# Kernel tuning notes

Hardware: AMD Instinct MI355X
Metric: run time of the kernel (lower is better)

Reference implementation:

```python
import jax, jax.numpy as jnp
import numpy as np
import math


def _sinusoidal_pe(seq_len, hidden_dim, dtype):
    pos = jnp.arange(seq_len, dtype=jnp.float32)[:, None]              # [S,1]
    div = jnp.exp(jnp.arange(0, hidden_dim, 2, dtype=jnp.float32) * (-math.log(10000.0) / hidden_dim))  # [H/2]
    ang = pos * div                                                    # [S,H/2]
    pe = jnp.stack([jnp.sin(ang), jnp.cos(ang)], axis=-1).reshape(seq_len, hidden_dim)  # interleave sin/cos
    return pe.astype(dtype)


def setup_inputs() -> dict:
    key = jax.random.key(0)
    ks = jax.random.split(key, 12)
    B, S, H = 4, 2048, 1024
    scale = 1.0 / math.sqrt(H)
    inp = {
        "x": jax.random.normal(ks[0], (B, S, H), dtype=jnp.float32),
        "mask": jax.random.randint(ks[1], (B, S, S), 0, 2, dtype=jnp.int32),
        "Wq": jax.random.normal(ks[2], (H, H), dtype=jnp.float32) * scale,
        "bq": jax.random.normal(ks[3], (H,), dtype=jnp.float32) * 0.02,
        "Wk": jax.random.normal(ks[4], (H, H), dtype=jnp.float32) * scale,
        "bk": jax.random.normal(ks[5], (H,), dtype=jnp.float32) * 0.02,
        "Wv": jax.random.normal(ks[6], (H, H), dtype=jnp.float32) * scale,
        "bv": jax.random.normal(ks[7], (H,), dtype=jnp.float32) * 0.02,
        "pos_bias": jax.random.normal(ks[8], (S, S), dtype=jnp.float32),
        "Wo": jax.random.normal(ks[9], (H, H), dtype=jnp.float32) * scale,
        "bo": jax.random.normal(ks[10], (H,), dtype=jnp.float32) * 0.02,
        "gamma": jnp.ones((H,), dtype=jnp.float32),
        "beta": jnp.zeros((H,), dtype=jnp.float32),
    }
    return inp


def reference(x, mask, Wq, bq, Wk, bk, Wv, bv, pos_bias, Wo, bo, gamma, beta):
    B, S, H = x.shape
    scale = math.sqrt(H)
    pe = _sinusoidal_pe(S, H, x.dtype)                  # [S,H]
    xp = x + pe[None, :, :]                             # [B,S,H]
    # torch Linear: y = x @ W.T + b
    q = jnp.einsum('bsh,oh->bso', xp, Wq) + bq
    k = jnp.einsum('bsh,oh->bso', xp, Wk) + bk
    v = jnp.einsum('bsh,oh->bso', xp, Wv) + bv
    scores = jnp.einsum('bqh,bkh->bqk', q, k) / scale   # [B,S,S]
    scores = scores + pos_bias[None, :S, :S]
    scores = jnp.where(mask == 0, jnp.asarray(-1e9, scores.dtype), scores)
    attn = jax.nn.softmax(scores, axis=-1)              # dropout = identity (eval mode)
    context = jnp.einsum('bqk,bkh->bqh', attn, v)
    out = jnp.einsum('bsh,oh->bso', context, Wo) + bo
    # LayerNorm(out + x)
    h = out + x
    mu = jnp.mean(h, axis=-1, keepdims=True)
    var = jnp.var(h, axis=-1, keepdims=True)
    normed = (h - mu) * jax.lax.rsqrt(var + 1e-5) * gamma + beta
    return normed, attn
```

## Files before the change

kernel.cpp:

```cpp
#include <hip/hip_runtime.h>
#include <hip/hip_bf16.h>
#include <math.h>

typedef __hip_bfloat16 bf16;
typedef __bf16 bf16x8 __attribute__((ext_vector_type(8)));
typedef float f32x4 __attribute__((ext_vector_type(4)));

static constexpr int  B_  = 4, S_ = 2048, H_ = 1024;
static constexpr long BSH = (long)B_ * S_ * H_;
static constexpr long SH  = (long)S_ * H_;
static constexpr long SS  = (long)S_ * S_;
static constexpr long HH  = (long)H_ * H_;

#define GLOAD_LDS16(gp, lp)                                                          \
  __builtin_amdgcn_global_load_lds((__attribute__((address_space(1))) void*)(gp),    \
                                   (__attribute__((address_space(3))) void*)(lp),    \
                                   16, 0, 0)

__device__ __forceinline__ float wave_reduce_sum(float v) {
#pragma unroll
  for (int o = 32; o; o >>= 1) v += __shfl_xor(v, o, 64);
  return v;
}
__device__ __forceinline__ float bf16r(float v) {
  return __bfloat162float(__float2bfloat16(v));
}

__global__ void prep_kernel(const float* __restrict__ Wq, const float* __restrict__ Wk,
                            const float* __restrict__ Wv, const float* __restrict__ Wo,
                            bf16* __restrict__ wdst,
                            const float* __restrict__ x, bf16* __restrict__ xpb,
                            const int* __restrict__ mask, unsigned* __restrict__ mask_bits) {
  const int bx  = blockIdx.x;
  const int tid = threadIdx.x;
  if (bx < 4096) {
    const int w = bx >> 10;
    const float* src = (w == 0) ? Wq : (w == 1) ? Wk : (w == 2) ? Wv : Wo;
    bf16* d = wdst + (long)w * HH;
    const int idx = ((bx & 1023) << 8) + tid;
    const float4 f = ((const float4*)src)[idx];
    d[idx * 4 + 0] = __float2bfloat16(f.x);
    d[idx * 4 + 1] = __float2bfloat16(f.y);
    d[idx * 4 + 2] = __float2bfloat16(f.z);
    d[idx * 4 + 3] = __float2bfloat16(f.w);
  } else if (bx < 20480) {
    const long idx = (((long)(bx - 4096)) << 8) + tid;
    const int  i   = (int)(idx & (H_ / 2 - 1));
    const long bs  = idx >> 9;
    const int  s   = (int)(bs & (S_ - 1));
    const float div = __expf((float)(2 * i) * (-9.210340371976184f / (float)H_));
    const float ang = (float)s * div;
    const float2 xv = ((const float2*)x)[idx];
    xpb[idx * 2 + 0] = __float2bfloat16(xv.x + __sinf(ang));
    xpb[idx * 2 + 1] = __float2bfloat16(xv.y + __cosf(ang));
  } else {
    const long uidx = (((long)(bx - 20480)) << 8) + tid;
    const int4* mp  = (const int4*)mask + uidx * 8;
    unsigned bits = 0;
#pragma unroll
    for (int q = 0; q < 8; ++q) {
      const int4 v = mp[q];
      bits |= (v.x ? 1u : 0u) << (q * 4 + 0);
      bits |= (v.y ? 1u : 0u) << (q * 4 + 1);
      bits |= (v.z ? 1u : 0u) << (q * 4 + 2);
      bits |= (v.w ? 1u : 0u) << (q * 4 + 3);
    }
    mask_bits[uidx] = bits;
  }
}

template <int MODE>
__global__ void gemm_nt(const bf16* __restrict__ A, long sA,
                        const bf16* __restrict__ Bm, long sB,
                        bf16* __restrict__ Cb, float* __restrict__ Cf, long sC,
                        int M, int N, int K,
                        const float* __restrict__ bias0,
                        const float* __restrict__ bias1,
                        const float* __restrict__ bias2,
                        const float* __restrict__ pos_bias,
                        const unsigned* __restrict__ mask_bits,
                        const float* __restrict__ xres,
                        const float* __restrict__ inv_sum) {
  constexpr int BM = 128, BN = 128, BK = 64;
  __shared__ bf16 As[BM * BK];
  __shared__ bf16 Bs[BN * BK];

  const int tid  = threadIdx.x;
  const int lane = tid & 63;
  const int wave = tid >> 6;
  const int wm   = wave & 1;
  const int wn   = wave >> 1;
  const int z    = blockIdx.z;
  const int m0   = blockIdx.x * BM;
  const int n0   = blockIdx.y * BN;

  const bf16* Ab = A  + (long)z * sA;
  const bf16* Bb = Bm + (long)z * sB;

  const int rw = tid >> 3;
  const int cp = (tid & 7) ^ (rw & 7);
  const bf16* ga = Ab + (long)(m0 + rw) * K + cp * 8;
  const bf16* gb = Bb + (long)(n0 + rw) * K + cp * 8;
  bf16* la = As + tid * 8;
  bf16* lb = Bs + tid * 8;

  f32x4 acc[4][4] = {};

  const int fr     = lane & 15;
  const int k0slot = lane >> 4;
  const int sw     = fr & 7;

  for (int k0 = 0; k0 < K; k0 += BK) {
#pragma unroll
    for (int q = 0; q < 4; ++q) {
      GLOAD_LDS16(ga + (long)(32 * q) * K + k0, la + q * 2048);
      GLOAD_LDS16(gb + (long)(32 * q) * K + k0, lb + q * 2048);
    }
    __syncthreads();
#pragma unroll
    for (int ks = 0; ks < 2; ++ks) {
      const int co = ((k0slot + 4 * ks) ^ sw) << 4;
      bf16x8 af[4], bfv[4];
#pragma unroll
      for (int i = 0; i < 4; ++i) {
        af[i]  = *(const bf16x8*)((const char*)As + (wm * 64 + i * 16 + fr) * 128 + co);
        bfv[i] = *(const bf16x8*)((const char*)Bs + (wn * 64 + i * 16 + fr) * 128 + co);
      }
#pragma unroll
      for (int i = 0; i < 4; ++i)
#pragma unroll
        for (int j = 0; j < 4; ++j)
          acc[i][j] = __builtin_amdgcn_mfma_f32_16x16x32_bf16(af[i], bfv[j], acc[i][j], 0, 0, 0);
    }
    __syncthreads();
  }

  const float* biasz = (MODE == 0) ? ((z == 0) ? bias0 : (z == 1) ? bias1 : bias2) : bias0;

  const int cc = lane & 15;
  const int cr = (lane >> 4) * 4;
#pragma unroll
  for (int i = 0; i < 4; ++i) {
    const int rowb = m0 + wm * 64 + i * 16 + cr;
#pragma unroll
    for (int j = 0; j < 4; ++j) {
      const int col = n0 + wn * 64 + j * 16 + cc;
#pragma unroll
      for (int r = 0; r < 4; ++r) {
        const int  row  = rowb + r;
        const long loff = (long)row * N + col;
        const long off  = (long)z * sC + loff;
        const float v   = acc[i][j][r];
        if (MODE == 0) {
          Cb[off] = __float2bfloat16(v + biasz[col]);
        } else if (MODE == 1) {
          const unsigned mw = mask_bits[off >> 5];
          float sc = v * (1.0f / 32.0f) + pos_bias[loff];
          if (((mw >> (col & 31)) & 1u) == 0u) sc = -1e9f;
          Cb[off] = __float2bfloat16(__expf(fminf(sc, 60.0f)));
        } else if (MODE == 2) {
          Cb[off] = __float2bfloat16(v * inv_sum[z * S_ + row]);
        } else {
          Cf[off] = v + biasz[col] + xres[off];
        }
      }
    }
  }
}

__global__ void transpose_kernel(const bf16* __restrict__ v, bf16* __restrict__ vT) {
  __shared__ bf16 tile[64][65];
  const int b     = blockIdx.z;
  const int sBase = blockIdx.x * 64;
  const int hBase = blockIdx.y * 64;
  const bf16* vb  = v  + (long)b * SH;
  bf16*       vTb = vT + (long)b * SH;
  const int tx = threadIdx.x & 63;
  const int ty = threadIdx.x >> 6;
#pragma unroll
  for (int r = ty; r < 64; r += 4)
    tile[r][tx] = vb[(long)(sBase + r) * H_ + hBase + tx];
  __syncthreads();
#pragma unroll
  for (int r = ty; r < 64; r += 4)
    vTb[(long)(hBase + r) * S_ + sBase + tx] = tile[tx][r];
}

__global__ void rownorm_kernel(const bf16* __restrict__ E, float* __restrict__ attn_f,
                               float* __restrict__ inv_sum) {
  const long row = blockIdx.x;
  const int  tid = threadIdx.x;
  const uint4 d = *(const uint4*)(E + row * (long)S_ + tid * 8);
  float ev[8];
  ev[0] = __uint_as_float(d.x << 16); ev[1] = __uint_as_float(d.x & 0xffff0000u);
  ev[2] = __uint_as_float(d.y << 16); ev[3] = __uint_as_float(d.y & 0xffff0000u);
  ev[4] = __uint_as_float(d.z << 16); ev[5] = __uint_as_float(d.z & 0xffff0000u);
  ev[6] = __uint_as_float(d.w << 16); ev[7] = __uint_as_float(d.w & 0xffff0000u);
  float s = 0.f;
#pragma unroll
  for (int i = 0; i < 8; ++i) s += ev[i];
  s = wave_reduce_sum(s);
  __shared__ float red[4];
  if ((tid & 63) == 0) red[tid >> 6] = s;
  __syncthreads();
  const float inv = 1.0f / fmaxf(red[0] + red[1] + red[2] + red[3], 1e-30f);
  if (tid == 0) inv_sum[row] = inv;
  float4 o0, o1;
  o0.x = bf16r(ev[0] * inv); o0.y = bf16r(ev[1] * inv);
  o0.z = bf16r(ev[2] * inv); o0.w = bf16r(ev[3] * inv);
  o1.x = bf16r(ev[4] * inv); o1.y = bf16r(ev[5] * inv);
  o1.z = bf16r(ev[6] * inv); o1.w = bf16r(ev[7] * inv);
  float4* dst = (float4*)(attn_f + row * (long)S_ + tid * 8);
  dst[0] = o0;
  dst[1] = o1;
}

__global__ void ln_kernel(float* __restrict__ h, const float* __restrict__ gamma,
                          const float* __restrict__ beta) {
  const long row = blockIdx.x;
  float* hr = h + row * (long)H_;
  const int tid = threadIdx.x;
  float v[4];
  float s = 0.f;
#pragma unroll
  for (int i = 0; i < 4; ++i) { v[i] = hr[tid + i * 256]; s += v[i]; }
  s = wave_reduce_sum(s);
  __shared__ float redA[4], redB[4];
  if ((tid & 63) == 0) redA[tid >> 6] = s;
  __syncthreads();
  const float mu = (redA[0] + redA[1] + redA[2] + redA[3]) * (1.0f / H_);
  float vs = 0.f;
#pragma unroll
  for (int i = 0; i < 4; ++i) { const float d = v[i] - mu; vs += d * d; }
  vs = wave_reduce_sum(vs);
  if ((tid & 63) == 0) redB[tid >> 6] = vs;
  __syncthreads();
  const float var  = (redB[0] + redB[1] + redB[2] + redB[3]) * (1.0f / H_);
  const float rstd = rsqrtf(var + 1e-5f);
#pragma unroll
  for (int i = 0; i < 4; ++i) {
    const int c = tid + i * 256;
    hr[c] = bf16r((v[i] - mu) * rstd * gamma[c] + beta[c]);
  }
}

extern "C" void kernel_launch(void* const* d_in, const int* in_sizes, int n_in,
                              void* d_out, int out_size, void* d_ws, size_t ws_size,
                              hipStream_t stream) {
  const float* x        = (const float*)d_in[0];
  const int*   mask     = (const int*)d_in[1];
  const float* Wq       = (const float*)d_in[2];
  const float* bq       = (const float*)d_in[3];
  const float* Wk       = (const float*)d_in[4];
  const float* bk       = (const float*)d_in[5];
  const float* Wv       = (const float*)d_in[6];
  const float* bv       = (const float*)d_in[7];
  const float* pos_bias = (const float*)d_in[8];
  const float* Wo       = (const float*)d_in[9];
  const float* bo       = (const float*)d_in[10];
  const float* gamma    = (const float*)d_in[11];
  const float* beta     = (const float*)d_in[12];

  float* normed_f = (float*)d_out;
  float* attn_f   = (float*)((char*)d_out + ((size_t)32 << 20));

  const size_t MiB = (size_t)1 << 20;
  bf16*     xpb       = (bf16*)d_ws;
  bf16*     q_b       = (bf16*)((char*)d_ws +  16 * MiB);
  bf16*     kbuf      = (bf16*)((char*)d_ws +  32 * MiB);
  bf16*     vbuf      = (bf16*)((char*)d_ws +  48 * MiB);
  bf16*     vT        = (bf16*)((char*)d_ws +  64 * MiB);
  bf16*     ctx       = (bf16*)((char*)d_ws +  80 * MiB);
  bf16*     attn_b    = (bf16*)((char*)d_ws +  96 * MiB);
  bf16*     wts       = (bf16*)((char*)d_ws + 128 * MiB);
  float*    inv_sum   = (float*)((char*)d_ws + 136 * MiB);
  unsigned* mask_bits = (unsigned*)((char*)d_ws + 137 * MiB);
  bf16* Wqb = wts, *Wob = wts + 3 * HH;

  const int MQKV = B_ * S_;

  prep_kernel<<<dim3(22528), 256, 0, stream>>>(Wq, Wk, Wv, Wo, wts, x, xpb,
                                               mask, mask_bits);

  gemm_nt<0><<<dim3(64, 8, 3), 256, 0, stream>>>(xpb, 0, Wqb, HH, q_b, nullptr, BSH,
                                                 MQKV, H_, H_, bq, bk, bv,
                                                 nullptr, nullptr, nullptr, nullptr);

  transpose_kernel<<<dim3(S_ / 64, H_ / 64, B_), 256, 0, stream>>>(vbuf, vT);

  gemm_nt<1><<<dim3(16, 16, B_), 256, 0, stream>>>(q_b, SH, kbuf, SH,
                                                   attn_b, nullptr, SS,
                                                   S_, S_, H_, nullptr, nullptr, nullptr,
                                                   pos_bias, mask_bits, nullptr, nullptr);

  rownorm_kernel<<<B_ * S_, 256, 0, stream>>>(attn_b, attn_f, inv_sum);

  gemm_nt<2><<<dim3(16, 8, B_), 256, 0, stream>>>(attn_b, SS, vT, SH,
                                                  ctx, nullptr, SH,
                                                  S_, H_, S_, nullptr, nullptr, nullptr,
                                                  nullptr, nullptr, nullptr, inv_sum);

  gemm_nt<3><<<dim3(64, 8, 1), 256, 0, stream>>>(ctx, 0, Wob, 0, nullptr, normed_f, 0,
                                                 MQKV, H_, H_, bo, nullptr, nullptr,
                                                 nullptr, nullptr, x, nullptr);

  ln_kernel<<<B_ * S_, 256, 0, stream>>>(normed_f, gamma, beta);
}
```

Measured before the change: 433.2 us.

## Double-buffer GEMM LDS tiles with async global-to-LDS prefetch

Converts the GEMM main loop to double-buffered LDS, issuing the next K-tile's global_load_lds before computing the current tile and waiting with explicit vmcnt counters. This hides global memory latency behind MFMA work instead of stalling at each tile load. It doubles LDS use to 64KB per block, which may reduce occupancy, and relies on hand-written waitcnt and barrier ordering.

```diff
diff --git a/kernel.cpp b/kernel.cpp
--- a/kernel.cpp
+++ b/kernel.cpp
@@ -16,6 +16,13 @@
   __builtin_amdgcn_global_load_lds((__attribute__((address_space(1))) void*)(gp),    \
                                    (__attribute__((address_space(3))) void*)(lp),    \
                                    16, 0, 0)
+
+#define BARRIER() do { __builtin_amdgcn_s_barrier(); asm volatile("" ::: "memory"); } while (0)
+
+template <int N> __device__ __forceinline__ void waitcnt_vm() {
+  if constexpr (N == 0)      asm volatile("s_waitcnt vmcnt(0)" ::: "memory");
+  else if constexpr (N == 8) asm volatile("s_waitcnt vmcnt(8)" ::: "memory");
+}
 
 __device__ __forceinline__ float wave_reduce_sum(float v) {
 #pragma unroll
@@ -82,8 +89,8 @@
                         const float* __restrict__ xres,
                         const float* __restrict__ inv_sum) {
   constexpr int BM = 128, BN = 128, BK = 64;
-  __shared__ bf16 As[BM * BK];
-  __shared__ bf16 Bs[BN * BK];
+  __shared__ bf16 As[2][BM * BK];
+  __shared__ bf16 Bs[2][BN * BK];
 
   const int tid  = threadIdx.x;
   const int lane = tid & 63;
@@ -101,8 +108,15 @@
   const int cp = (tid & 7) ^ (rw & 7);
   const bf16* ga = Ab + (long)(m0 + rw) * K + cp * 8;
   const bf16* gb = Bb + (long)(n0 + rw) * K + cp * 8;
-  bf16* la = As + tid * 8;
-  bf16* lb = Bs + tid * 8;
+
+  auto stage = [&](int tile, int buf) {
+    const long k0 = (long)tile * BK;
+#pragma unroll
+    for (int q = 0; q < 4; ++q) {
+      GLOAD_LDS16(ga + (long)(32 * q) * K + k0, &As[buf][tid * 8 + q * 2048]);
+      GLOAD_LDS16(gb + (long)(32 * q) * K + k0, &Bs[buf][tid * 8 + q * 2048]);
+    }
+  };
 
   f32x4 acc[4][4] = {};
 
@@ -110,21 +124,27 @@
   const int k0slot = lane >> 4;
   const int sw     = fr & 7;
 
-  for (int k0 = 0; k0 < K; k0 += BK) {
-#pragma unroll
-    for (int q = 0; q < 4; ++q) {
-      GLOAD_LDS16(ga + (long)(32 * q) * K + k0, la + q * 2048);
-      GLOAD_LDS16(gb + (long)(32 * q) * K + k0, lb + q * 2048);
-    }
-    __syncthreads();
+  const int nkt = K / BK;
+  stage(0, 0);
+  for (int kt = 0; kt < nkt; ++kt) {
+    const int cur = kt & 1;
+    if (kt + 1 < nkt) {
+      stage(kt + 1, cur ^ 1);
+      waitcnt_vm<8>();
+    } else {
+      waitcnt_vm<0>();
+    }
+    BARRIER();
+    const char* bAc = (const char*)&As[cur][0];
+    const char* bBc = (const char*)&Bs[cur][0];
 #pragma unroll
     for (int ks = 0; ks < 2; ++ks) {
       const int co = ((k0slot + 4 * ks) ^ sw) << 4;
       bf16x8 af[4], bfv[4];
 #pragma unroll
       for (int i = 0; i < 4; ++i) {
-        af[i]  = *(const bf16x8*)((const char*)As + (wm * 64 + i * 16 + fr) * 128 + co);
-        bfv[i] = *(const bf16x8*)((const char*)Bs + (wn * 64 + i * 16 + fr) * 128 + co);
+        af[i]  = *(const bf16x8*)(bAc + (wm * 64 + i * 16 + fr) * 128 + co);
+        bfv[i] = *(const bf16x8*)(bBc + (wn * 64 + i * 16 + fr) * 128 + co);
       }
 #pragma unroll
       for (int i = 0; i < 4; ++i)
@@ -132,7 +152,7 @@
         for (int j = 0; j < 4; ++j)
           acc[i][j] = __builtin_amdgcn_mfma_f32_16x16x32_bf16(af[i], bfv[j], acc[i][j], 0, 0, 0);
     }
-    __syncthreads();
+    BARRIER();
   }
 
   const float* biasz = (MODE == 0) ? ((z == 0) ? bias0 : (z == 1) ? bias1 : bias2) : bias0;
```

Measured after the change: 430.3 us. No clear change (-0.7%).
